# Kernel tuning notes

Hardware: AMD Instinct MI355X
Metric: run time of the kernel (lower is better)

The kernel has to match this reference:

```python
import jax, jax.numpy as jnp
import numpy as np
import math

B, T, D, H = 2, 4096, 2048, 16
HD = D // H  # 128
OFFSET = -math.log(math.sqrt(D)) + 1e-6  # q_offset == k_offset in the original


def setup_inputs() -> dict:
    key = jax.random.key(0)
    ks = jax.random.split(key, 7)
    s = 1.0 / np.sqrt(D).astype(np.float32)  # keep exp() in a sane range
    return {
        "hidden_states": jax.random.normal(ks[0], (B, T, D), jnp.float32),
        "Wq": jax.random.normal(ks[1], (D, D), jnp.float32) * s,
        "Wk": jax.random.normal(ks[2], (D, D), jnp.float32) * s,
        "Wv": jax.random.normal(ks[3], (D, D), jnp.float32) * s,
        "Wo": jax.random.normal(ks[4], (D, D), jnp.float32) * s,
        "Fq": jax.random.normal(ks[5], (D, D), jnp.float32) * s,  # q feature map
        "Fk": jax.random.normal(ks[6], (D, D), jnp.float32) * s,  # k feature map
    }


def _split_heads(x):
    # [B, T, D] -> [B, H, T, HD]
    return x.reshape(B, T, H, HD).transpose(0, 2, 1, 3)


def reference(hidden_states, Wq, Wk, Wv, Wo, Fq, Fk):
    q = hidden_states @ Wq
    k = hidden_states @ Wk
    v = hidden_states @ Wv
    # Performer-style positive feature maps
    q_prime = jnp.exp(q @ Fq + OFFSET)
    k_prime = jnp.exp(k @ Fk + OFFSET)
    q_p = _split_heads(q_prime)   # [B,H,T,HD]
    k_p = _split_heads(k_prime)
    v_h = _split_heads(v)
    # causal_attention1: q_t^T (k_t v_t^T) == (q_t . k_t) * v_t, then cumsum over T.
    # Equivalent to the original [B,H,T,HD,HD] outer-product + cumsum, without
    # materializing the huge intermediate.
    dot = jnp.einsum("bhtd,bhtd->bht", q_p, k_p)           # [B,H,T]
    att_raw = jnp.cumsum(dot[..., None] * v_h, axis=2)      # [B,H,T,HD]
    attn = att_raw / k_p                                    # att_norm = k_prime
    # merge heads: [B,H,T,HD] -> [B,T,D]
    attn = attn.transpose(0, 2, 1, 3).reshape(B, T, D)
    return attn @ Wo
```

## Files before the change

kernel.cpp:

```cpp
#include <hip/hip_runtime.h>
#include <hip/hip_bf16.h>
#include <cmath>

constexpr int Bc = 2, Tc = 4096, Dc = 2048, Hc = 16, HDc = 128;
constexpr int Mrows = Bc * Tc;
constexpr int NCHUNK = 32, CHUNK = 128;

__device__ __forceinline__ unsigned short f2bf(float x) {
  union { float f; unsigned int u; } v; v.f = x;
  unsigned int r = v.u + 0x7FFFu + ((v.u >> 16) & 1u);
  return (unsigned short)(r >> 16);
}
__device__ __forceinline__ float bf2f(unsigned short u) {
  union { unsigned int i; float f; } v; v.i = ((unsigned int)u) << 16;
  return v.f;
}

typedef __attribute__((ext_vector_type(8))) short bf16x8;
typedef __attribute__((ext_vector_type(4))) float f32x4;

__device__ __forceinline__ void gload16(const unsigned short* g, unsigned short* l) {
  __builtin_amdgcn_global_load_lds(
      (const __attribute__((address_space(1))) void*)(const void*)g,
      (__attribute__((address_space(3))) void*)(void*)l,
      16, 0, 0);
}

__global__ void cvt_bf16(const float* __restrict__ in, unsigned short* __restrict__ outp) {
  size_t i = ((size_t)blockIdx.x * 256 + threadIdx.x) * 4;
  float4 f = *(const float4*)(in + i);
  ushort4 u;
  u.x = f2bf(f.x); u.y = f2bf(f.y); u.z = f2bf(f.z); u.w = f2bf(f.w);
  *(ushort4*)(outp + i) = u;
}

__global__ void cvt_bf16_2(const float* __restrict__ in0, unsigned short* __restrict__ out0,
                           const float* __restrict__ in1, unsigned short* __restrict__ out1) {
  const float* in = blockIdx.y ? in1 : in0;
  unsigned short* op = blockIdx.y ? out1 : out0;
  size_t i = ((size_t)blockIdx.x * 256 + threadIdx.x) * 4;
  float4 f = *(const float4*)(in + i);
  ushort4 u;
  u.x = f2bf(f.x); u.y = f2bf(f.y); u.z = f2bf(f.z); u.w = f2bf(f.w);
  *(ushort4*)(op + i) = u;
}

__global__ void transpose_cvt4(const float* __restrict__ W0, unsigned short* __restrict__ T0,
                               const float* __restrict__ W1, unsigned short* __restrict__ T1,
                               const float* __restrict__ W2, unsigned short* __restrict__ T2,
                               const float* __restrict__ W3, unsigned short* __restrict__ T3) {
  const float* W; unsigned short* Wt;
  switch (blockIdx.z) {
    case 0: W = W0; Wt = T0; break;
    case 1: W = W1; Wt = T1; break;
    case 2: W = W2; Wt = T2; break;
    default: W = W3; Wt = T3; break;
  }
  __shared__ float tile[32][33];
  int n0 = blockIdx.x * 32, k0 = blockIdx.y * 32;
  int tx = threadIdx.x & 31, ty = threadIdx.x >> 5;
#pragma unroll
  for (int i = 0; i < 4; ++i)
    tile[ty + 8 * i][tx] = W[(size_t)(k0 + ty + 8 * i) * Dc + n0 + tx];
  __syncthreads();
#pragma unroll
  for (int i = 0; i < 4; ++i)
    Wt[(size_t)(n0 + ty + 8 * i) * Dc + k0 + tx] = f2bf(tile[tx][ty + 8 * i]);
}

template <int EPI, int WMw, int WNw, int MI, int NI>
__global__ __launch_bounds__(WMw * WNw * 64, 2) void gemmL(
    const unsigned short* __restrict__ A0, const unsigned short* __restrict__ B0,
    void* __restrict__ C0, void* __restrict__ C1, void* __restrict__ C2,
    const unsigned short* __restrict__ A1, const unsigned short* __restrict__ B1,
    void* __restrict__ C1a,
    int M, int N, int lda, int ldc, float eoff) {
  constexpr int K = 2048;
  constexpr int NT = K / 32;
  constexpr int THREADS = WMw * WNw * 64;
  constexpr int BM = WMw * MI * 16;
  constexpr int BN = WNw * NI * 16;
  constexpr int ASLAB = BM * 32;
  constexpr int BSLAB = BN * 32;
  constexpr int BUF = ASLAB + BSLAB;
  constexpr int SROWS = THREADS / 4;
  static_assert(2 * SROWS == BM && BM == BN, "staging geometry");
  extern __shared__ unsigned short lds[];

  const unsigned short* A = A0;
  const unsigned short* Bt = B0;
  void* Cz = C0;
  if (blockIdx.y) { A = A1; Bt = B1; Cz = C1a; }

  const int tid = threadIdx.x;
  const int lane = tid & 63;
  const int wave = tid >> 6;
  const int wm = wave / WNw;
  const int wn = wave % WNw;

  const int nbn = N / BN;
  const int nwg = (M / BM) * nbn;
  const int bidx = (int)blockIdx.x;
  const int wgid = (bidx & 7) * (nwg >> 3) + (bidx >> 3);
  const int bm = wgid / nbn;
  const int bn = wgid % nbn;

  const int srow = tid >> 2;
  const int scolL = (tid & 3) << 3;
  const int scolG = scolL ^ ((srow & 6) << 2);
  const unsigned short* gA = A + (size_t)(bm * BM + srow) * lda + scolG;
  const unsigned short* gB = Bt + (size_t)(bn * BN + srow) * K + scolG;
  const int sstage = srow * 32 + scolL;
  const size_t arstep = (size_t)SROWS * lda;
  const size_t brstep = (size_t)SROWS * K;

  const int fr = lane & 15;
  const int fko = ((lane >> 4) << 3) ^ ((lane & 6) << 2);
  const int aoff = (wm * MI * 16 + fr) * 32 + fko;
  const int boff = ASLAB + (wn * NI * 16 + fr) * 32 + fko;

  f32x4 acc[MI][NI] = {};

#pragma unroll
  for (int t = 0; t < 3; ++t) {
    const unsigned short* sA = gA + t * 32;
    const unsigned short* sB = gB + t * 32;
    unsigned short* dst = lds + t * BUF;
    gload16(sA,          dst + sstage);
    gload16(sA + arstep, dst + sstage + SROWS * 32);
    gload16(sB,          dst + ASLAB + sstage);
    gload16(sB + brstep, dst + ASLAB + sstage + SROWS * 32);
  }
  asm volatile("s_waitcnt vmcnt(8)" ::: "memory");
  __builtin_amdgcn_s_barrier();

  for (int v = 0; v < NT; ++v) {
    const int rb = (v & 3) * BUF;
    const int wb = ((v + 3) & 3) * BUF;
    const int tn = (v + 3) & (NT - 1);
    const unsigned short* srcA = gA + tn * 32;
    const unsigned short* srcB = gB + tn * 32;

    bf16x8 af[MI], bfv[NI];
#pragma unroll
    for (int mi = 0; mi < MI; ++mi)
      af[mi] = *(const bf16x8*)(lds + rb + aoff + mi * 512);
#pragma unroll
    for (int ni = 0; ni < NI; ++ni)
      bfv[ni] = *(const bf16x8*)(lds + rb + boff + ni * 512);

    gload16(srcA,          lds + wb + sstage);
    gload16(srcA + arstep, lds + wb + sstage + SROWS * 32);
    gload16(srcB,          lds + wb + ASLAB + sstage);
    gload16(srcB + brstep, lds + wb + ASLAB + sstage + SROWS * 32);

    __builtin_amdgcn_s_setprio(1);
#pragma unroll
    for (int mi = 0; mi < MI; ++mi)
#pragma unroll
      for (int ni = 0; ni < NI; ++ni)
        acc[mi][ni] = __builtin_amdgcn_mfma_f32_16x16x32_bf16(af[mi], bfv[ni], acc[mi][ni], 0, 0, 0);
    __builtin_amdgcn_s_setprio(0);

    asm volatile("s_waitcnt vmcnt(8)" ::: "memory");
    __builtin_amdgcn_s_barrier();
  }

  const int fq = lane >> 4;
  const int crow = bm * BM + wm * (MI * 16);
  if constexpr (EPI == 3) {
    const int seg = bn >> 3;
    unsigned short* outp = (unsigned short*)(seg == 0 ? C0 : (seg == 1 ? C1 : C2));
    const int ccol = (bn & 7) * BN + wn * (NI * 16) + fr;
#pragma unroll
    for (int mi = 0; mi < MI; ++mi)
#pragma unroll
      for (int ni = 0; ni < NI; ++ni)
#pragma unroll
        for (int ii = 0; ii < 4; ++ii) {
          const int r = crow + mi * 16 + fq * 4 + ii;
          const int c = ccol + ni * 16;
          float vv = acc[mi][ni][ii];
          if (seg < 2) vv = __expf(vv + eoff);
          outp[(size_t)r * ldc + c] = f2bf(vv);
        }
  } else {
    const int ccol = bn * BN + wn * (NI * 16) + fr;
#pragma unroll
    for (int mi = 0; mi < MI; ++mi)
#pragma unroll
      for (int ni = 0; ni < NI; ++ni)
#pragma unroll
        for (int ii = 0; ii < 4; ++ii) {
          const int r = crow + mi * 16 + fq * 4 + ii;
          const int c = ccol + ni * 16;
          const size_t idx = (size_t)r * ldc + c;
          float vv = acc[mi][ni][ii];
          if (EPI == 0) ((float*)Cz)[idx] = vv;
          else          ((unsigned short*)Cz)[idx] = f2bf(vv);
        }
  }
}

__global__ void dot_chunks(const unsigned short* __restrict__ qp,
                           const unsigned short* __restrict__ kp,
                           const unsigned short* __restrict__ v,
                           float* __restrict__ dotb,
                           float* __restrict__ chks) {
  __shared__ float dt[CHUNK];
  const int bid = blockIdx.x;
  const int c = bid & (NCHUNK - 1);
  const int bh = bid >> 5;
  const int b = bh >> 4, h = bh & 15;
  const int tid = threadIdx.x;
  const int lane = tid & 63, wv = tid >> 6;
  const int qw = lane >> 4, j = lane & 15;
  const int t0 = c * CHUNK;

#pragma unroll
  for (int pass = 0; pass < 8; ++pass) {
    const int tl = pass * 16 + wv * 4 + qw;
    const int t = t0 + tl;
    const size_t base = ((size_t)(b * Tc + t)) * Dc + h * HDc + j * 8;
    bf16x8 q = *(const bf16x8*)(qp + base);
    bf16x8 k = *(const bf16x8*)(kp + base);
    float p = 0.f;
#pragma unroll
    for (int i = 0; i < 8; ++i)
      p += bf2f((unsigned short)q[i]) * bf2f((unsigned short)k[i]);
#pragma unroll
    for (int m = 8; m; m >>= 1) p += __shfl_xor(p, m);
    if (j == 0) {
      dt[tl] = p;
      dotb[(size_t)bh * Tc + t] = p;
    }
  }
  __syncthreads();
  if (tid < HDc) {
    const int d = tid;
    const unsigned short* vp = v + ((size_t)(b * Tc + t0)) * Dc + h * HDc + d;
    float acc = 0.f;
    for (int t = 0; t < CHUNK; ++t)
      acc += dt[t] * bf2f(vp[(size_t)t * Dc]);
    chks[(size_t)bid * HDc + d] = acc;
  }
}

__global__ void scan_offsets(float* __restrict__ chks) {
  int bh = blockIdx.x;
  int d = threadIdx.x;
  float run = 0.f;
  for (int c = 0; c < NCHUNK; ++c) {
    size_t idx = ((size_t)bh * NCHUNK + c) * HDc + d;
    float tmp = chks[idx];
    chks[idx] = run;
    run += tmp;
  }
}

__global__ void scan_final(const float* __restrict__ dotb,
                           const unsigned short* __restrict__ v,
                           const unsigned short* __restrict__ kp,
                           const float* __restrict__ chks,
                           unsigned short* __restrict__ attn) {
  int bid = blockIdx.x;
  int c = bid % NCHUNK, bh = bid / NCHUNK;
  int b = bh / Hc, h = bh % Hc;
  int d = threadIdx.x;
  const float* dp = dotb + (size_t)bh * Tc + c * CHUNK;
  size_t base = ((size_t)(b * Tc + c * CHUNK)) * Dc + h * HDc + d;
  float acc = chks[(size_t)bid * HDc + d];
  for (int t = 0; t < CHUNK; ++t) {
    size_t idx = base + (size_t)t * Dc;
    acc += dp[t] * bf2f(v[idx]);
    attn[idx] = f2bf(acc / bf2f(kp[idx]));
  }
}

extern "C" void kernel_launch(void* const* d_in, const int* in_sizes, int n_in,
                              void* d_out, int out_size, void* d_ws, size_t ws_size,
                              hipStream_t stream) {
  const float* hs = (const float*)d_in[0];
  const float* Wq = (const float*)d_in[1];
  const float* Wk = (const float*)d_in[2];
  const float* Wv = (const float*)d_in[3];
  const float* Wo = (const float*)d_in[4];
  const float* Fq = (const float*)d_in[5];
  const float* Fk = (const float*)d_in[6];
  float* out = (float*)d_out;

  const size_t MD = (size_t)Mrows * Dc;
  const size_t DD = (size_t)Dc * Dc;

  char* w = (char*)d_ws;
  size_t off = 0;
  auto take = [&](size_t bytes) -> void* {
    void* r = w + off;
    off += (bytes + 255) & ~(size_t)255;
    return r;
  };

  unsigned short* hs_bf = (unsigned short*)take(MD * 2);
  unsigned short* wq_bf = (unsigned short*)take(DD * 2);
  unsigned short* wtfq  = (unsigned short*)take(DD * 2);
  unsigned short* wk_bf = (unsigned short*)take(DD * 2);
  unsigned short* wtfk  = (unsigned short*)take(DD * 2);
  unsigned short* wcat  = (unsigned short*)take(3 * DD * 2);
  unsigned short* wto   = (unsigned short*)take(DD * 2);
  unsigned short* Kp    = (unsigned short*)take(MD * 2);
  unsigned short* Vbf   = (unsigned short*)take(MD * 2);
  float* dotb = (float*)take((size_t)Bc * Hc * Tc * 4);
  float* chks = (float*)take((size_t)Bc * Hc * NCHUNK * HDc * 4);

  unsigned short* Qp = wq_bf;
  unsigned short* attnbf = hs_bf;

  const float OFF = (float)(-0.5 * log(2048.0) + 1e-6);

  (void)hipFuncSetAttribute((const void*)gemmL<0, 2, 4, 8, 4>, hipFuncAttributeMaxDynamicSharedMemorySize, 131072);
  (void)hipFuncSetAttribute((const void*)gemmL<3, 2, 4, 8, 4>, hipFuncAttributeMaxDynamicSharedMemorySize, 131072);
  (void)hipFuncSetAttribute((const void*)gemmL<1, 2, 2, 4, 4>, hipFuncAttributeMaxDynamicSharedMemorySize, 65536);

  cvt_bf16<<<(int)(MD / 1024), 256, 0, stream>>>(hs, hs_bf);
  cvt_bf16_2<<<dim3((int)(DD / 1024), 2), 256, 0, stream>>>(Wq, wq_bf, Wk, wk_bf);

  transpose_cvt4<<<dim3(Dc / 32, Dc / 32, 4), 256, 0, stream>>>(
      Fq, wtfq, Fk, wtfk, Wv, wcat + 2 * DD, Wo, wto);

  gemmL<1, 2, 2, 4, 4><<<dim3(256, 2), 256, 65536, stream>>>(
      wtfq, wq_bf, wcat, nullptr, nullptr,
      wtfk, wk_bf, wcat + DD,
      2048, 2048, 2048, 2048, 0.f);

  const int fblocks = (Mrows / 256) * (6144 / 256);
  gemmL<3, 2, 4, 8, 4><<<fblocks, 512, 131072, stream>>>(
      hs_bf, wcat, Qp, Kp, Vbf, nullptr, nullptr, nullptr,
      Mrows, 6144, Dc, Dc, OFF);

  dot_chunks<<<Bc * Hc * NCHUNK, 256, 0, stream>>>(Qp, Kp, Vbf, dotb, chks);

  scan_offsets<<<Bc * Hc, 128, 0, stream>>>(chks);
  scan_final<<<Bc * Hc * NCHUNK, 128, 0, stream>>>(dotb, Vbf, Kp, chks, attnbf);

  const int gblocks = (Mrows / 256) * (Dc / 256);
  gemmL<0, 2, 4, 8, 4><<<gblocks, 512, 131072, stream>>>(
      attnbf, wto, out, nullptr, nullptr, nullptr, nullptr, nullptr,
      Mrows, Dc, Dc, Dc, 0.f);
}
```

Measured before the change: 426.9 us.

## Pre-pack B weights into MFMA panels and load B fragments directly to registers

After: 450.8 us. 5.6% more time.

```diff
diff --git a/kernel.cpp b/kernel.cpp
--- a/kernel.cpp
+++ b/kernel.cpp
@@ -18,6 +18,10 @@
 
 typedef __attribute__((ext_vector_type(8))) short bf16x8;
 typedef __attribute__((ext_vector_type(4))) float f32x4;
+
+__device__ __forceinline__ size_t poff(int n, int k) {
+  return ((size_t)((n >> 4) * 64 + (k >> 5)) << 9) + (size_t)((n & 15) * 32 + (k & 31));
+}
 
 __device__ __forceinline__ void gload16(const unsigned short* g, unsigned short* l) {
   __builtin_amdgcn_global_load_lds(
@@ -34,27 +38,32 @@
   *(ushort4*)(outp + i) = u;
 }
 
-__global__ void cvt_bf16_2(const float* __restrict__ in0, unsigned short* __restrict__ out0,
-                           const float* __restrict__ in1, unsigned short* __restrict__ out1) {
-  const float* in = blockIdx.y ? in1 : in0;
-  unsigned short* op = blockIdx.y ? out1 : out0;
-  size_t i = ((size_t)blockIdx.x * 256 + threadIdx.x) * 4;
-  float4 f = *(const float4*)(in + i);
-  ushort4 u;
-  u.x = f2bf(f.x); u.y = f2bf(f.y); u.z = f2bf(f.z); u.w = f2bf(f.w);
-  *(ushort4*)(op + i) = u;
-}
-
-__global__ void transpose_cvt4(const float* __restrict__ W0, unsigned short* __restrict__ T0,
+__global__ void panelize_cvt2(const float* __restrict__ in0, unsigned short* __restrict__ out0,
+                              const float* __restrict__ in1, unsigned short* __restrict__ out1) {
+  const float* in = blockIdx.z ? in1 : in0;
+  unsigned short* op = blockIdx.z ? out1 : out0;
+  const int n = blockIdx.x * 16 + (threadIdx.x >> 4);
+  const int k = blockIdx.y * 128 + (threadIdx.x & 15) * 8;
+  float4 f0 = *(const float4*)(in + (size_t)n * Dc + k);
+  float4 f1 = *(const float4*)(in + (size_t)n * Dc + k + 4);
+  bf16x8 u;
+  u[0] = (short)f2bf(f0.x); u[1] = (short)f2bf(f0.y);
+  u[2] = (short)f2bf(f0.z); u[3] = (short)f2bf(f0.w);
+  u[4] = (short)f2bf(f1.x); u[5] = (short)f2bf(f1.y);
+  u[6] = (short)f2bf(f1.z); u[7] = (short)f2bf(f1.w);
+  *(bf16x8*)(op + poff(n, k)) = u;
+}
+
+__global__ void transpose_mix4(const float* __restrict__ W0, unsigned short* __restrict__ T0,
                                const float* __restrict__ W1, unsigned short* __restrict__ T1,
                                const float* __restrict__ W2, unsigned short* __restrict__ T2,
                                const float* __restrict__ W3, unsigned short* __restrict__ T3) {
-  const float* W; unsigned short* Wt;
+  const float* W; unsigned short* Wt; bool pan;
   switch (blockIdx.z) {
-    case 0: W = W0; Wt = T0; break;
-    case 1: W = W1; Wt = T1; break;
-    case 2: W = W2; Wt = T2; break;
-    default: W = W3; Wt = T3; break;
+    case 0: W = W0; Wt = T0; pan = false; break;
+    case 1: W = W1; Wt = T1; pan = false; break;
+    case 2: W = W2; Wt = T2; pan = true; break;
+    default: W = W3; Wt = T3; pan = true; break;
   }
   __shared__ float tile[32][33];
   int n0 = blockIdx.x * 32, k0 = blockIdx.y * 32;
@@ -64,12 +73,16 @@
     tile[ty + 8 * i][tx] = W[(size_t)(k0 + ty + 8 * i) * Dc + n0 + tx];
   __syncthreads();
 #pragma unroll
-  for (int i = 0; i < 4; ++i)
-    Wt[(size_t)(n0 + ty + 8 * i) * Dc + k0 + tx] = f2bf(tile[tx][ty + 8 * i]);
+  for (int i = 0; i < 4; ++i) {
+    const int n = n0 + ty + 8 * i, k = k0 + tx;
+    unsigned short v = f2bf(tile[tx][ty + 8 * i]);
+    if (pan) Wt[poff(n, k)] = v;
+    else     Wt[(size_t)n * Dc + k] = v;
+  }
 }
 
 template <int EPI, int WMw, int WNw, int MI, int NI>
-__global__ __launch_bounds__(WMw * WNw * 64, 2) void gemmL(
+__global__ __launch_bounds__(WMw * WNw * 64, 2) void gemmB(
     const unsigned short* __restrict__ A0, const unsigned short* __restrict__ B0,
     void* __restrict__ C0, void* __restrict__ C1, void* __restrict__ C2,
     const unsigned short* __restrict__ A1, const unsigned short* __restrict__ B1,
@@ -81,10 +94,11 @@
   constexpr int BM = WMw * MI * 16;
   constexpr int BN = WNw * NI * 16;
   constexpr int ASLAB = BM * 32;
-  constexpr int BSLAB = BN * 32;
-  constexpr int BUF = ASLAB + BSLAB;
   constexpr int SROWS = THREADS / 4;
-  static_assert(2 * SROWS == BM && BM == BN, "staging geometry");
+  constexpr int APASS = BM / SROWS;
+  static_assert(BM % SROWS == 0, "staging geometry");
+  static_assert(NI == 4, "vmcnt ledger assumes 4 B loads/tile");
+  static_assert(APASS == 2, "vmcnt ledger assumes 2 A gloads/tile");
   extern __shared__ unsigned short lds[];
 
   const unsigned short* A = A0;
@@ -109,62 +123,66 @@
   const int scolL = (tid & 3) << 3;
   const int scolG = scolL ^ ((srow & 6) << 2);
   const unsigned short* gA = A + (size_t)(bm * BM + srow) * lda + scolG;
-  const unsigned short* gB = Bt + (size_t)(bn * BN + srow) * K + scolG;
   const int sstage = srow * 32 + scolL;
   const size_t arstep = (size_t)SROWS * lda;
-  const size_t brstep = (size_t)SROWS * K;
 
   const int fr = lane & 15;
   const int fko = ((lane >> 4) << 3) ^ ((lane & 6) << 2);
   const int aoff = (wm * MI * 16 + fr) * 32 + fko;
-  const int boff = ASLAB + (wn * NI * 16 + fr) * 32 + fko;
+
+  const int bcol = ((EPI == 3) ? (bn & 7) : bn) * BN + wn * (NI * 16);
+  const unsigned short* gBp = Bt
+      + ((EPI == 3) ? (size_t)(bn >> 3) * ((size_t)Dc * Dc) : 0)
+      + ((size_t)(bcol >> 4) << 15)
+      + (size_t)(fr * 32 + ((lane >> 4) << 3));
 
   f32x4 acc[MI][NI] = {};
-
-#pragma unroll
-  for (int t = 0; t < 3; ++t) {
-    const unsigned short* sA = gA + t * 32;
-    const unsigned short* sB = gB + t * 32;
-    unsigned short* dst = lds + t * BUF;
-    gload16(sA,          dst + sstage);
-    gload16(sA + arstep, dst + sstage + SROWS * 32);
-    gload16(sB,          dst + ASLAB + sstage);
-    gload16(sB + brstep, dst + ASLAB + sstage + SROWS * 32);
-  }
+  bf16x8 bA_[NI], bB_[NI];
+
+#pragma unroll
+  for (int t = 0; t < 3; ++t)
+#pragma unroll
+    for (int p = 0; p < APASS; ++p)
+      gload16(gA + t * 32 + p * arstep, lds + t * ASLAB + sstage + p * SROWS * 32);
+#pragma unroll
+  for (int ni = 0; ni < NI; ++ni)
+    bA_[ni] = *(const bf16x8*)(gBp + ((size_t)ni << 15));
   asm volatile("s_waitcnt vmcnt(8)" ::: "memory");
   __builtin_amdgcn_s_barrier();
 
-  for (int v = 0; v < NT; ++v) {
-    const int rb = (v & 3) * BUF;
-    const int wb = ((v + 3) & 3) * BUF;
-    const int tn = (v + 3) & (NT - 1);
-    const unsigned short* srcA = gA + tn * 32;
-    const unsigned short* srcB = gB + tn * 32;
-
-    bf16x8 af[MI], bfv[NI];
-#pragma unroll
-    for (int mi = 0; mi < MI; ++mi)
-      af[mi] = *(const bf16x8*)(lds + rb + aoff + mi * 512);
-#pragma unroll
-    for (int ni = 0; ni < NI; ++ni)
-      bfv[ni] = *(const bf16x8*)(lds + rb + boff + ni * 512);
-
-    gload16(srcA,          lds + wb + sstage);
-    gload16(srcA + arstep, lds + wb + sstage + SROWS * 32);
-    gload16(srcB,          lds + wb + ASLAB + sstage);
-    gload16(srcB + brstep, lds + wb + ASLAB + sstage + SROWS * 32);
-
-    __builtin_amdgcn_s_setprio(1);
-#pragma unroll
-    for (int mi = 0; mi < MI; ++mi)
-#pragma unroll
-      for (int ni = 0; ni < NI; ++ni)
-        acc[mi][ni] = __builtin_amdgcn_mfma_f32_16x16x32_bf16(af[mi], bfv[ni], acc[mi][ni], 0, 0, 0);
-    __builtin_amdgcn_s_setprio(0);
-
-    asm volatile("s_waitcnt vmcnt(8)" ::: "memory");
-    __builtin_amdgcn_s_barrier();
-  }
+#define TB(V, BC, BN_)                                                          \
+  {                                                                             \
+    const int rb = ((V) & 3) * ASLAB;                                           \
+    const int wb = (((V) + 3) & 3) * ASLAB;                                     \
+    const int tb = ((V) + 1) & (NT - 1);                                        \
+    const int ta = ((V) + 3) & (NT - 1);                                        \
+    bf16x8 af[MI];                                                              \
+    _Pragma("unroll")                                                           \
+    for (int mi = 0; mi < MI; ++mi)                                             \
+      af[mi] = *(const bf16x8*)(lds + rb + aoff + mi * 512);                    \
+    _Pragma("unroll")                                                           \
+    for (int ni = 0; ni < NI; ++ni)                                             \
+      BN_[ni] = *(const bf16x8*)(gBp + ((size_t)ni << 15) + tb * 512);          \
+    _Pragma("unroll")                                                           \
+    for (int p = 0; p < APASS; ++p)                                             \
+      gload16(gA + ta * 32 + p * arstep, lds + wb + sstage + p * SROWS * 32);   \
+    __builtin_amdgcn_s_setprio(1);                                              \
+    _Pragma("unroll")                                                           \
+    for (int mi = 0; mi < MI; ++mi)                                             \
+      _Pragma("unroll")                                                         \
+      for (int ni = 0; ni < NI; ++ni)                                           \
+        acc[mi][ni] = __builtin_amdgcn_mfma_f32_16x16x32_bf16(                  \
+            af[mi], BC[ni], acc[mi][ni], 0, 0, 0);                              \
+    __builtin_amdgcn_s_setprio(0);                                              \
+    asm volatile("s_waitcnt vmcnt(8)" ::: "memory");         \
+    __builtin_amdgcn_s_barrier();                                               \
+  }
+
+  for (int v = 0; v < NT; v += 2) {
+    TB(v, bA_, bB_)
+    TB(v + 1, bB_, bA_)
+  }
+#undef TB
 
   const int fq = lane >> 4;
   const int crow = bm * BM + wm * (MI * 16);
@@ -183,6 +201,19 @@
           float vv = acc[mi][ni][ii];
           if (seg < 2) vv = __expf(vv + eoff);
           outp[(size_t)r * ldc + c] = f2bf(vv);
+        }
+  } else if constexpr (EPI == 4) {
+    unsigned short* outp = (unsigned short*)Cz;
+    const int ccol = bn * BN + wn * (NI * 16) + fr;
+#pragma unroll
+    for (int mi = 0; mi < MI; ++mi)
+#pragma unroll
+      for (int ni = 0; ni < NI; ++ni)
+#pragma unroll
+        for (int ii = 0; ii < 4; ++ii) {
+          const int r = crow + mi * 16 + fq * 4 + ii;
+          const int c = ccol + ni * 16;
+          outp[poff(r, c)] = f2bf(acc[mi][ni][ii]);
         }
   } else {
     const int ccol = bn * BN + wn * (NI * 16) + fr;
@@ -301,39 +332,39 @@
   };
 
   unsigned short* hs_bf = (unsigned short*)take(MD * 2);
-  unsigned short* wq_bf = (unsigned short*)take(DD * 2);
-  unsigned short* wtfq  = (unsigned short*)take(DD * 2);
-  unsigned short* wk_bf = (unsigned short*)take(DD * 2);
-  unsigned short* wtfk  = (unsigned short*)take(DD * 2);
-  unsigned short* wcat  = (unsigned short*)take(3 * DD * 2);
-  unsigned short* wto   = (unsigned short*)take(DD * 2);
-  unsigned short* Kp    = (unsigned short*)take(MD * 2);
-  unsigned short* Vbf   = (unsigned short*)take(MD * 2);
+  unsigned short* wqP  = (unsigned short*)take(DD * 2);
+  unsigned short* wtfq = (unsigned short*)take(DD * 2);
+  unsigned short* wkP  = (unsigned short*)take(DD * 2);
+  unsigned short* wtfk = (unsigned short*)take(DD * 2);
+  unsigned short* wcat = (unsigned short*)take(3 * DD * 2);
+  unsigned short* woP  = (unsigned short*)take(DD * 2);
+  unsigned short* Kp   = (unsigned short*)take(MD * 2);
+  unsigned short* Vbf  = (unsigned short*)take(MD * 2);
   float* dotb = (float*)take((size_t)Bc * Hc * Tc * 4);
   float* chks = (float*)take((size_t)Bc * Hc * NCHUNK * HDc * 4);
 
-  unsigned short* Qp = wq_bf;
+  unsigned short* Qp = wqP;
   unsigned short* attnbf = hs_bf;
 
   const float OFF = (float)(-0.5 * log(2048.0) + 1e-6);
 
-  (void)hipFuncSetAttribute((const void*)gemmL<0, 2, 4, 8, 4>, hipFuncAttributeMaxDynamicSharedMemorySize, 131072);
-  (void)hipFuncSetAttribute((const void*)gemmL<3, 2, 4, 8, 4>, hipFuncAttributeMaxDynamicSharedMemorySize, 131072);
-  (void)hipFuncSetAttribute((const void*)gemmL<1, 2, 2, 4, 4>, hipFuncAttributeMaxDynamicSharedMemorySize, 65536);
+  (void)hipFuncSetAttribute((const void*)gemmB<0, 2, 4, 8, 4>, hipFuncAttributeMaxDynamicSharedMemorySize, 65536);
+  (void)hipFuncSetAttribute((const void*)gemmB<3, 2, 4, 8, 4>, hipFuncAttributeMaxDynamicSharedMemorySize, 65536);
+  (void)hipFuncSetAttribute((const void*)gemmB<4, 2, 2, 4, 4>, hipFuncAttributeMaxDynamicSharedMemorySize, 32768);
 
   cvt_bf16<<<(int)(MD / 1024), 256, 0, stream>>>(hs, hs_bf);
-  cvt_bf16_2<<<dim3((int)(DD / 1024), 2), 256, 0, stream>>>(Wq, wq_bf, Wk, wk_bf);
-
-  transpose_cvt4<<<dim3(Dc / 32, Dc / 32, 4), 256, 0, stream>>>(
-      Fq, wtfq, Fk, wtfk, Wv, wcat + 2 * DD, Wo, wto);
-
-  gemmL<1, 2, 2, 4, 4><<<dim3(256, 2), 256, 65536, stream>>>(
-      wtfq, wq_bf, wcat, nullptr, nullptr,
-      wtfk, wk_bf, wcat + DD,
+  panelize_cvt2<<<dim3(Dc / 16, Dc / 128, 2), 256, 0, stream>>>(Wq, wqP, Wk, wkP);
+
+  transpose_mix4<<<dim3(Dc / 32, Dc / 32, 4), 256, 0, stream>>>(
+      Fq, wtfq, Fk, wtfk, Wv, wcat + 2 * DD, Wo, woP);
+
+  gemmB<4, 2, 2, 4, 4><<<dim3(256, 2), 256, 32768, stream>>>(
+      wtfq, wqP, wcat, nullptr, nullptr,
+      wtfk, wkP, wcat + DD,
       2048, 2048, 2048, 2048, 0.f);
 
   const int fblocks = (Mrows / 256) * (6144 / 256);
-  gemmL<3, 2, 4, 8, 4><<<fblocks, 512, 131072, stream>>>(
+  gemmB<3, 2, 4, 8, 4><<<fblocks, 512, 65536, stream>>>(
       hs_bf, wcat, Qp, Kp, Vbf, nullptr, nullptr, nullptr,
       Mrows, 6144, Dc, Dc, OFF);
 
@@ -343,7 +374,7 @@
   scan_final<<<Bc * Hc * NCHUNK, 128, 0, stream>>>(dotb, Vbf, Kp, chks, attnbf);
 
   const int gblocks = (Mrows / 256) * (Dc / 256);
-  gemmL<0, 2, 4, 8, 4><<<gblocks, 512, 131072, stream>>>(
-      attnbf, wto, out, nullptr, nullptr, nullptr, nullptr, nullptr,
+  gemmB<0, 2, 4, 8, 4><<<gblocks, 512, 65536, stream>>>(
+      attnbf, woP, out, nullptr, nullptr, nullptr, nullptr, nullptr,
       Mrows, Dc, Dc, Dc, 0.f);
 }
```

## Fuse q·k dot into projection GEMM via summed exp(q+k) feature weights

Applied to the files above, without the earlier changes.

After: 419.8 us. Within noise of the previous version (-1.7%).

```diff
diff --git a/kernel.cpp b/kernel.cpp
--- a/kernel.cpp
+++ b/kernel.cpp
@@ -5,6 +5,7 @@
 constexpr int Bc = 2, Tc = 4096, Dc = 2048, Hc = 16, HDc = 128;
 constexpr int Mrows = Bc * Tc;
 constexpr int NCHUNK = 32, CHUNK = 128;
+constexpr int BHT = Bc * Hc * Tc;
 
 __device__ __forceinline__ unsigned short f2bf(float x) {
   union { float f; unsigned int u; } v; v.f = x;
@@ -43,6 +44,16 @@
   ushort4 u;
   u.x = f2bf(f.x); u.y = f2bf(f.y); u.z = f2bf(f.z); u.w = f2bf(f.w);
   *(ushort4*)(op + i) = u;
+}
+
+__global__ void add_bf16(unsigned short* __restrict__ dst, const unsigned short* __restrict__ src) {
+  size_t i = ((size_t)blockIdx.x * 256 + threadIdx.x) * 8;
+  bf16x8 a = *(const bf16x8*)(dst + i);
+  bf16x8 b = *(const bf16x8*)(src + i);
+#pragma unroll
+  for (int j = 0; j < 8; ++j)
+    a[j] = (short)f2bf(bf2f((unsigned short)a[j]) + bf2f((unsigned short)b[j]));
+  *(bf16x8*)(dst + i) = a;
 }
 
 __global__ void transpose_cvt4(const float* __restrict__ W0, unsigned short* __restrict__ T0,
@@ -168,22 +179,54 @@
 
   const int fq = lane >> 4;
   const int crow = bm * BM + wm * (MI * 16);
-  if constexpr (EPI == 3) {
+  if constexpr (EPI == 5) {
     const int seg = bn >> 3;
-    unsigned short* outp = (unsigned short*)(seg == 0 ? C0 : (seg == 1 ? C1 : C2));
-    const int ccol = (bn & 7) * BN + wn * (NI * 16) + fr;
-#pragma unroll
-    for (int mi = 0; mi < MI; ++mi)
-#pragma unroll
-      for (int ni = 0; ni < NI; ++ni)
+    if (seg == 0) {
+      float s2[MI][4];
+#pragma unroll
+      for (int mi = 0; mi < MI; ++mi)
 #pragma unroll
         for (int ii = 0; ii < 4; ++ii) {
-          const int r = crow + mi * 16 + fq * 4 + ii;
-          const int c = ccol + ni * 16;
-          float vv = acc[mi][ni][ii];
-          if (seg < 2) vv = __expf(vv + eoff);
-          outp[(size_t)r * ldc + c] = f2bf(vv);
+          float t = 0.f;
+#pragma unroll
+          for (int ni = 0; ni < NI; ++ni)
+            t += __expf(acc[mi][ni][ii] + 2.f * eoff);
+          s2[mi][ii] = t;
         }
+#pragma unroll
+      for (int m = 1; m < 16; m <<= 1)
+#pragma unroll
+        for (int mi = 0; mi < MI; ++mi)
+#pragma unroll
+          for (int ii = 0; ii < 4; ++ii)
+            s2[mi][ii] += __shfl_xor(s2[mi][ii], m);
+      const int h = (bn & 7) * 2 + (wn >> 1);
+      const int part = wn & 1;
+      float* dp = (float*)C0 + (size_t)part * BHT;
+#pragma unroll
+      for (int u = 0; u < 2; ++u) {
+        const int idx = fr * 2 + u;
+        const int mi = idx >> 2, ii = idx & 3;
+        const int r = crow + mi * 16 + fq * 4 + ii;
+        const int b = r >> 12, t = r & (Tc - 1);
+        dp[((size_t)(b * Hc + h)) * Tc + t] = s2[mi][ii];
+      }
+    } else {
+      unsigned short* outp = (unsigned short*)(seg == 1 ? C1 : C2);
+      const int ccol = (bn & 7) * BN + wn * (NI * 16) + fr;
+#pragma unroll
+      for (int mi = 0; mi < MI; ++mi)
+#pragma unroll
+        for (int ni = 0; ni < NI; ++ni)
+#pragma unroll
+          for (int ii = 0; ii < 4; ++ii) {
+            const int r = crow + mi * 16 + fq * 4 + ii;
+            const int c = ccol + ni * 16;
+            float vv = acc[mi][ni][ii];
+            if (seg == 1) vv = __expf(vv + eoff);
+            outp[(size_t)r * ldc + c] = f2bf(vv);
+          }
+    }
   } else {
     const int ccol = bn * BN + wn * (NI * 16) + fr;
 #pragma unroll
@@ -202,48 +245,29 @@
   }
 }
 
-__global__ void dot_chunks(const unsigned short* __restrict__ qp,
-                           const unsigned short* __restrict__ kp,
-                           const unsigned short* __restrict__ v,
-                           float* __restrict__ dotb,
-                           float* __restrict__ chks) {
+__global__ void scan_chunks2(const float* __restrict__ dotP,
+                             const unsigned short* __restrict__ v,
+                             float* __restrict__ dotb,
+                             float* __restrict__ chks) {
   __shared__ float dt[CHUNK];
   const int bid = blockIdx.x;
   const int c = bid & (NCHUNK - 1);
   const int bh = bid >> 5;
   const int b = bh >> 4, h = bh & 15;
-  const int tid = threadIdx.x;
-  const int lane = tid & 63, wv = tid >> 6;
-  const int qw = lane >> 4, j = lane & 15;
+  const int d = threadIdx.x;
   const int t0 = c * CHUNK;
 
-#pragma unroll
-  for (int pass = 0; pass < 8; ++pass) {
-    const int tl = pass * 16 + wv * 4 + qw;
-    const int t = t0 + tl;
-    const size_t base = ((size_t)(b * Tc + t)) * Dc + h * HDc + j * 8;
-    bf16x8 q = *(const bf16x8*)(qp + base);
-    bf16x8 k = *(const bf16x8*)(kp + base);
-    float p = 0.f;
-#pragma unroll
-    for (int i = 0; i < 8; ++i)
-      p += bf2f((unsigned short)q[i]) * bf2f((unsigned short)k[i]);
-#pragma unroll
-    for (int m = 8; m; m >>= 1) p += __shfl_xor(p, m);
-    if (j == 0) {
-      dt[tl] = p;
-      dotb[(size_t)bh * Tc + t] = p;
-    }
-  }
+  const size_t di = (size_t)bh * Tc + t0 + d;
+  float dv = dotP[di] + dotP[(size_t)BHT + di];
+  dt[d] = dv;
+  dotb[di] = dv;
   __syncthreads();
-  if (tid < HDc) {
-    const int d = tid;
-    const unsigned short* vp = v + ((size_t)(b * Tc + t0)) * Dc + h * HDc + d;
-    float acc = 0.f;
-    for (int t = 0; t < CHUNK; ++t)
-      acc += dt[t] * bf2f(vp[(size_t)t * Dc]);
-    chks[(size_t)bid * HDc + d] = acc;
-  }
+
+  const unsigned short* vp = v + ((size_t)(b * Tc + t0)) * Dc + h * HDc + d;
+  float acc = 0.f;
+  for (int t = 0; t < CHUNK; ++t)
+    acc += dt[t] * bf2f(vp[(size_t)t * Dc]);
+  chks[(size_t)bid * HDc + d] = acc;
 }
 
 __global__ void scan_offsets(float* __restrict__ chks) {
@@ -309,16 +333,16 @@
   unsigned short* wto   = (unsigned short*)take(DD * 2);
   unsigned short* Kp    = (unsigned short*)take(MD * 2);
   unsigned short* Vbf   = (unsigned short*)take(MD * 2);
-  float* dotb = (float*)take((size_t)Bc * Hc * Tc * 4);
+  float* dotP = (float*)take((size_t)2 * BHT * 4);
+  float* dotb = (float*)take((size_t)BHT * 4);
   float* chks = (float*)take((size_t)Bc * Hc * NCHUNK * HDc * 4);
 
-  unsigned short* Qp = wq_bf;
   unsigned short* attnbf = hs_bf;
 
   const float OFF = (float)(-0.5 * log(2048.0) + 1e-6);
 
   (void)hipFuncSetAttribute((const void*)gemmL<0, 2, 4, 8, 4>, hipFuncAttributeMaxDynamicSharedMemorySize, 131072);
-  (void)hipFuncSetAttribute((const void*)gemmL<3, 2, 4, 8, 4>, hipFuncAttributeMaxDynamicSharedMemorySize, 131072);
+  (void)hipFuncSetAttribute((const void*)gemmL<5, 2, 4, 8, 4>, hipFuncAttributeMaxDynamicSharedMemorySize, 131072);
   (void)hipFuncSetAttribute((const void*)gemmL<1, 2, 2, 4, 4>, hipFuncAttributeMaxDynamicSharedMemorySize, 65536);
 
   cvt_bf16<<<(int)(MD / 1024), 256, 0, stream>>>(hs, hs_bf);
@@ -332,12 +356,14 @@
       wtfk, wk_bf, wcat + DD,
       2048, 2048, 2048, 2048, 0.f);
 
+  add_bf16<<<(int)(DD / 2048), 256, 0, stream>>>(wcat, wcat + DD);
+
   const int fblocks = (Mrows / 256) * (6144 / 256);
-  gemmL<3, 2, 4, 8, 4><<<fblocks, 512, 131072, stream>>>(
-      hs_bf, wcat, Qp, Kp, Vbf, nullptr, nullptr, nullptr,
+  gemmL<5, 2, 4, 8, 4><<<fblocks, 512, 131072, stream>>>(
+      hs_bf, wcat, dotP, Kp, Vbf, nullptr, nullptr, nullptr,
       Mrows, 6144, Dc, Dc, OFF);
 
-  dot_chunks<<<Bc * Hc * NCHUNK, 256, 0, stream>>>(Qp, Kp, Vbf, dotb, chks);
+  scan_chunks2<<<Bc * Hc * NCHUNK, 128, 0, stream>>>(dotP, Vbf, dotb, chks);
 
   scan_offsets<<<Bc * Hc, 128, 0, stream>>>(chks);
   scan_final<<<Bc * Hc * NCHUNK, 128, 0, stream>>>(dotb, Vbf, Kp, chks, attnbf);
```
